# Optimization experiments

Hardware: AMD Instinct MI355X
Metric: run time of the kernel (lower is better)

Reference implementation:

```python
import jax, jax.numpy as jnp
import numpy as np
from jax import lax

B, N, M, C = 32, 4096, 256, 91
EPS = 1e-7  # torchvision giou_loss eps
NEG_INF = -jnp.inf


def _make_boxes(key, b, n):
    # valid xyxy boxes in [0,1]
    kc, ks = jax.random.split(key)
    c = jax.random.uniform(kc, (b, n, 2), minval=0.1, maxval=0.9)
    wh = jax.random.uniform(ks, (b, n, 2), minval=0.02, maxval=0.2)
    return jnp.concatenate([c - wh / 2, c + wh / 2], axis=-1)


def setup_inputs() -> dict:
    key = jax.random.key(0)
    k1, k2, k3, k4 = jax.random.split(key, 4)
    return {
        "pr_boxes": _make_boxes(k1, B, N),
        "gt_boxes": _make_boxes(k2, B, M),
        "pr_class_logits": jax.random.normal(k3, (B, N, C), dtype=jnp.float32),
        "gt_classes": jax.random.randint(k4, (B, M), 0, C),
    }


def _box_iou(a, b):
    # a: [N,4], b: [M,4] xyxy -> [N,M] (torchvision.ops.box_iou)
    lt = jnp.maximum(a[:, None, :2], b[None, :, :2])
    rb = jnp.minimum(a[:, None, 2:], b[None, :, 2:])
    wh = jnp.clip(rb - lt, 0.0)
    inter = wh[..., 0] * wh[..., 1]
    area_a = (a[:, 2] - a[:, 0]) * (a[:, 3] - a[:, 1])
    area_b = (b[:, 2] - b[:, 0]) * (b[:, 3] - b[:, 1])
    union = area_a[:, None] + area_b[None, :] - inter
    return inter / union


def _match(pr, gt):
    # greedy maximal-IoU matching: sequentially take global argmax, mask row+col
    ious = _box_iou(pr, gt)  # [N, M]

    def step(ious, _):
        idx = jnp.argmax(ious)
        i, j = idx // M, idx % M
        ious = ious.at[i, :].set(NEG_INF).at[:, j].set(NEG_INF)
        return ious, (i, j)

    _, (pr_idx, gt_order) = lax.scan(step, ious, None, length=M)
    pr_mask = jnp.zeros((N,), dtype=bool).at[pr_idx].set(True)
    return pr_idx, gt_order, pr_mask


def _giou_loss_mean(b1, b2):
    # elementwise generalized_box_iou_loss, reduction='mean' (torchvision)
    xi1 = jnp.maximum(b1[:, 0], b2[:, 0])
    yi1 = jnp.maximum(b1[:, 1], b2[:, 1])
    xi2 = jnp.minimum(b1[:, 2], b2[:, 2])
    yi2 = jnp.minimum(b1[:, 3], b2[:, 3])
    inter = jnp.clip(xi2 - xi1, 0.0) * jnp.clip(yi2 - yi1, 0.0)
    area1 = (b1[:, 2] - b1[:, 0]) * (b1[:, 3] - b1[:, 1])
    area2 = (b2[:, 2] - b2[:, 0]) * (b2[:, 3] - b2[:, 1])
    union = area1 + area2 - inter
    iou = inter / (union + EPS)
    xc1 = jnp.minimum(b1[:, 0], b2[:, 0])
    yc1 = jnp.minimum(b1[:, 1], b2[:, 1])
    xc2 = jnp.maximum(b1[:, 2], b2[:, 2])
    yc2 = jnp.maximum(b1[:, 3], b2[:, 3])
    area_c = (xc2 - xc1) * (yc2 - yc1)
    giou = iou - (area_c - union) / (area_c + EPS)
    return jnp.mean(1.0 - giou)


def reference(pr_boxes, gt_boxes, pr_class_logits, gt_classes):
    pr_idx, gt_order, pr_mask = jax.vmap(_match)(pr_boxes, gt_boxes)  # [B,M],[B,M],[B,N]
    # unmatched prediction indices (fixed count N-M)
    neg_idx = jax.vmap(lambda m: jnp.nonzero(~m, size=N - M)[0])(pr_mask)  # [B, N-M]

    pr_pos = jnp.take_along_axis(pr_boxes, pr_idx[..., None], axis=1)   # [B,M,4]
    gt_pos = jnp.take_along_axis(gt_boxes, gt_order[..., None], axis=1)  # [B,M,4]
    pr_neg = jnp.take_along_axis(pr_boxes, neg_idx[..., None], axis=1)  # [B,N-M,4]
    gt_neg = jnp.zeros_like(pr_neg)

    l_loss = (jax.vmap(_giou_loss_mean)(pr_pos, gt_pos).sum()
              + jax.vmap(_giou_loss_mean)(pr_neg, gt_neg).sum())
    # c_loss is never accumulated in the original module (classification branch is dead code)
    c_loss = 0.0
    count = pr_boxes.shape[0]
    return (c_loss + l_loss) / count / 2.0
```

## Files before the change

### kernel.cpp

```cpp
#include <hip/hip_runtime.h>

#pragma clang fp contract(off)

#define NBOX 4096
#define MBOX 256
#define NBATCH 32
#define GEPS 1e-7f
#define DEPTH 12
#define RDEPTH 8

typedef unsigned long long u64;
typedef unsigned int u32;
typedef unsigned short u16;

#define OFF_PRS   0
#define OFF_TOP   65536
#define OFF_G     90112
#define OFF_GAR   94208
#define OFF_MATCH 95232
#define LDS_BYTES 96256

__device__ __forceinline__ u64 shfl_u64(u64 x, int src) {
  u32 lo = (u32)x, hi = (u32)(x >> 32);
  lo = __shfl(lo, src, 64);
  hi = __shfl(hi, src, 64);
  return ((u64)hi << 32) | (u64)lo;
}

__device__ __forceinline__ u32 wave_max_u32(u32 x) {
#define DPPL32(CTRL)                                                            \
  {                                                                             \
    u32 s = (u32)__builtin_amdgcn_update_dpp(0, (int)x, CTRL, 0xf, 0xf, true);  \
    x = x > s ? x : s;                                                          \
  }
  DPPL32(0xB1) DPPL32(0x4E) DPPL32(0x141) DPPL32(0x140) DPPL32(0x142) DPPL32(0x143)
#undef DPPL32
  return (u32)__builtin_amdgcn_readlane((int)x, 63);
}

__device__ __forceinline__ u64 wave_max_colkey(u64 key) {
  u32 iou = (u32)(key >> 13);
  u32 maxiou = wave_max_u32(iou);
  u32 tb = (iou == maxiou) ? ((u32)key & 0x1FFFu) : 0u;
  u32 maxtb = wave_max_u32(tb);
  return ((u64)maxiou << 13) | (u64)maxtb;
}

__device__ __forceinline__ u32 iou_bits(float4 a, float areaA, float4 g, float gar) {
  #pragma clang fp contract(off)
  float w = fminf(a.z, g.z) - fmaxf(a.x, g.x);
  float h = fminf(a.w, g.w) - fmaxf(a.y, g.y);
  w = fmaxf(w, 0.0f);
  h = fmaxf(h, 0.0f);
  float inter = w * h;
  float uni = (areaA + gar) - inter;
  float v = inter / uni;
  return __float_as_uint(v);
}

__device__ __forceinline__ float giou_loss(float ax1, float ay1, float ax2, float ay2,
                                           float bx1, float by1, float bx2, float by2) {
  #pragma clang fp contract(off)
  float xi1 = fmaxf(ax1, bx1), yi1 = fmaxf(ay1, by1);
  float xi2 = fminf(ax2, bx2), yi2 = fminf(ay2, by2);
  float inter = fmaxf(xi2 - xi1, 0.0f) * fmaxf(yi2 - yi1, 0.0f);
  float area1 = (ax2 - ax1) * (ay2 - ay1);
  float area2 = (bx2 - bx1) * (by2 - by1);
  float uni = (area1 + area2) - inter;
  float iou = inter / (uni + GEPS);
  float xc1 = fminf(ax1, bx1), yc1 = fminf(ay1, by1);
  float xc2 = fmaxf(ax2, bx2), yc2 = fmaxf(ay2, by2);
  float areac = (xc2 - xc1) * (yc2 - yc1);
  float giou = iou - (areac - uni) / (areac + GEPS);
  return 1.0f - giou;
}


__global__ __launch_bounds__(256) __attribute__((amdgpu_waves_per_eu(1, 6)))
void init_cols(const float4* __restrict__ pr, const float4* __restrict__ gt,
               u64* __restrict__ topG) {
  const int blk = blockIdx.x;
  const int b = blk >> 6, cg = blk & 63;
  const int tid = threadIdx.x, lane = tid & 63, wid = tid >> 6;
  const int j = cg * 4 + wid;
  const float4* prb = pr + (size_t)b * NBOX;
  float4 gb = gt[(size_t)b * MBOX + j];
  float gar = (gb.z - gb.x) * (gb.w - gb.y);

  u64 t0 = 0ull, t1 = 0ull, t2 = 0ull, dm = 0ull;
  for (int k = 0; k < 64; ++k) {
    int r = (k << 6) + lane;
    float4 a = prb[r];
    float areaA = (a.z - a.x) * (a.w - a.y);
    u64 key = ((u64)iou_bits(a, areaA, gb, gar) << 13) | (u64)(NBOX - r);
    bool c0 = key > t0, c1 = key > t1, c2 = key > t2;
    u64 d = c2 ? t2 : key;
    if (d > dm) dm = d;
    u64 n1 = c1 ? (c0 ? t0 : key) : t1;
    u64 n2 = c2 ? (c1 ? t1 : key) : t2;
    t0 = c0 ? key : t0;
    t1 = n1;
    t2 = n2;
  }
  u64* out = topG + ((size_t)b * MBOX + j) * DEPTH;
  int h = 0;
  u64 m12 = 0ull;
  for (int e = 0; e < DEPTH; ++e) {
    u64 cand = (h == 0) ? t0 : (h == 1) ? t1 : (h == 2) ? t2 : 0ull;
    u64 m = wave_max_colkey(cand);
    if (cand == m && m) h++;
    if (lane == 0) out[e] = m;
    m12 = m;
  }
  if (__ballot(dm > m12) != 0ull) {
    u64 t[DEPTH];
    #pragma unroll
    for (int q = 0; q < DEPTH; ++q) t[q] = 0ull;
    for (int k = 0; k < 64; ++k) {
      int r = (k << 6) + lane;
      float4 a = prb[r];
      float areaA = (a.z - a.x) * (a.w - a.y);
      u64 key = ((u64)iou_bits(a, areaA, gb, gar) << 13) | (u64)(NBOX - r);
      if (key > t[DEPTH - 1]) {
        t[DEPTH - 1] = key;
        #pragma unroll
        for (int q = DEPTH - 1; q > 0; --q)
          if (t[q] > t[q - 1]) { u64 tmp = t[q]; t[q] = t[q - 1]; t[q - 1] = tmp; }
      }
    }
    int h2 = 0;
    for (int e = 0; e < DEPTH; ++e) {
      u64 cand = 0;
      #pragma unroll
      for (int q = 0; q < DEPTH; ++q) if (q == h2) cand = t[q];
      u64 m = wave_max_colkey(cand);
      if (cand == m && m) h2++;
      if (lane == 0) out[e] = m;
    }
  }
}

__global__ __launch_bounds__(64) __attribute__((amdgpu_waves_per_eu(1, 4)))
void greedy_kernel(const float4* __restrict__ pr, const float4* __restrict__ gt,
                   const u64* __restrict__ topG, float* __restrict__ partial) {
  extern __shared__ char smem[];
  float4* prs  = (float4*)(smem + OFF_PRS);
  u64* top     = (u64*)(smem + OFF_TOP);
  float4* g    = (float4*)(smem + OFF_G);
  float* garea = (float*)(smem + OFF_GAR);
  u32* match   = (u32*)(smem + OFF_MATCH);

  const int b = blockIdx.x;
  const int lane = threadIdx.x;
  const float4* prb = pr + (size_t)b * NBOX;

  float negdiff = 0.0f, possum = 0.0f, negsub = 0.0f;
  for (int k = 0; k < 64; ++k) {
    int r = (k << 6) + lane;
    float4 a = prb[r];
    prs[r] = a;
    negdiff += giou_loss(a.x, a.y, a.z, a.w, 0.0f, 0.0f, 0.0f, 0.0f);
  }
  #pragma unroll
  for (int k = 0; k < 4; ++k) {
    int j = (k << 6) + lane;
    float4 gg = gt[(size_t)b * MBOX + j];
    g[j] = gg;
    garea[j] = (gg.z - gg.x) * (gg.w - gg.y);
  }
  {
    float4* dst = (float4*)top;
    const float4* src = (const float4*)(topG + (size_t)b * MBOX * DEPTH);
    for (int k = 0; k < MBOX * DEPTH / 2 / 64; ++k) dst[(k << 6) + lane] = src[(k << 6) + lane];
  }
  u64 rowlive = ~0ull;
  u64 cb[4];
  u64 la[4];
  u64 cfc[4];
  u32 posreg = 0x02020202u;
  #pragma unroll
  for (int q = 0; q < 4; ++q) {
    int j = (q << 6) + lane;
    cfc[q] = (u64)(MBOX - j);
    u64 e0 = top[j * DEPTH];
    u64 e1 = top[j * DEPTH + 1];
    cb[q] = ((e0 >> 13) << 22) | ((e0 & 0x1FFFull) << 9) | cfc[q];
    la[q] = e1;
  }

  for (int step = 0; step < MBOX; ++step) {
    u64 m0 = cb[0] > cb[1] ? cb[0] : cb[1];
    u64 m1 = cb[2] > cb[3] ? cb[2] : cb[3];
    u64 mb = m0 > m1 ? m0 : m1;
    u32 iou32 = (u32)(mb >> 22);
    u32 maxiou = wave_max_u32(iou32);
    u32 tb = (iou32 == maxiou) ? ((u32)mb & 0x3FFFFFu) : 0u;
    u32 maxtb = wave_max_u32(tb);
    if (lane == 0) match[step] = maxtb;
    if (step == MBOX - 1) break;
    const u32 rfield = (maxtb >> 9) & 0x1FFFu;
    const int i = NBOX - (int)rfield;
    u64 kill = (lane == (i & 63)) ? (1ull << (i >> 6)) : 0ull;
    rowlive &= ~kill;
    u32 walkmask = 0;
    #pragma unroll
    for (int q = 0; q < 4; ++q) {
      u32 lo22 = (u32)cb[q] & 0x3FFFFFu;
      bool aff = (lo22 >> 9) == rfield;
      bool ismatch = (lo22 == maxtb);
      if (aff && ismatch) cb[q] = 0ull;
      if (aff && !ismatch) walkmask |= (1u << q);
    }
    u64 wb = __ballot(walkmask != 0);
    if (wb != 0ull) {
      u32 need = walkmask;
      u32 exmask = 0;
      for (;;) {
        #pragma unroll
        for (int q = 0; q < 4; ++q) {
          u64 e = la[q];
          int r = NBOX - (int)(e & 0x1FFFull);
          u64 rl = shfl_u64(rowlive, r & 63);
          if ((need >> q) & 1) {
            if (e == 0ull) {
              cb[q] = 0ull;
              need &= ~(1u << q);
              exmask |= (1u << q);
            } else if ((rl >> ((r >> 6) & 63)) & 1ull) {
              cb[q] = ((e >> 13) << 22) | ((e & 0x1FFFull) << 9) | cfc[q];
              need &= ~(1u << q);
              int p = (int)((posreg >> (q * 8)) & 0xFFu);
              la[q] = (p < DEPTH) ? top[((q << 6) + lane) * DEPTH + p] : 0ull;
              posreg = (posreg & ~(0xFFu << (q * 8))) | ((u32)(p + 1) << (q * 8));
            } else {
              int p = (int)((posreg >> (q * 8)) & 0xFFu);
              la[q] = (p < DEPTH) ? top[((q << 6) + lane) * DEPTH + p] : 0ull;
              posreg = (posreg & ~(0xFFu << (q * 8))) | ((u32)(p + 1) << (q * 8));
            }
          }
        }
        if (__ballot(need != 0) == 0ull) break;
      }
      u64 exb = __ballot(exmask != 0);
      while (exb != 0ull) {
        const int src = (int)__ffsll((unsigned long long)exb) - 1;
        const u32 em = (u32)__shfl((int)exmask, src, 64);
        const int q = __ffs(em) - 1;
        const int jj = (q << 6) + src;
        if (lane == src) exmask &= ~(1u << q);
        exb = __ballot(exmask != 0);
        float4 gb = g[jj];
        float gar = garea[jj];
        u64 t[RDEPTH];
        #pragma unroll
        for (int z = 0; z < RDEPTH; ++z) t[z] = 0ull;
        for (int k = 0; k < 64; ++k) {
          if ((rowlive >> k) & 1ull) {
            int rr = (k << 6) + lane;
            float4 a = prs[rr];
            float areaA = (a.z - a.x) * (a.w - a.y);
            u64 key = ((u64)iou_bits(a, areaA, gb, gar) << 13) | (u64)(NBOX - rr);
            if (key > t[RDEPTH - 1]) {
              t[RDEPTH - 1] = key;
              #pragma unroll
              for (int z = RDEPTH - 1; z > 0; --z)
                if (t[z] > t[z - 1]) { u64 tmp = t[z]; t[z] = t[z - 1]; t[z - 1] = tmp; }
            }
          }
        }
        u64 ent0 = 0ull, ent1 = 0ull;
        int h = 0;
        for (int e = 0; e < RDEPTH; ++e) {
          u64 cand = 0;
          #pragma unroll
          for (int z = 0; z < RDEPTH; ++z) if (z == h) cand = t[z];
          u64 mm = wave_max_colkey(cand);
          if (cand == mm && mm) h++;
          if (e == 0) ent0 = mm;
          if (e == 1) ent1 = mm;
          if (lane == 0) top[jj * DEPTH + e] = mm;
        }
        if (lane >= RDEPTH && lane < DEPTH) top[jj * DEPTH + lane] = 0ull;
        if (lane == src) {
          cb[q] = ((ent0 >> 13) << 22) | ((ent0 & 0x1FFFull) << 9) | cfc[q];
          la[q] = ent1;
          posreg = (posreg & ~(0xFFu << (q * 8))) | (2u << (q * 8));
        }
      }
    }
  }

  #pragma unroll
  for (int t4 = 0; t4 < 4; ++t4) {
    int s = (t4 << 6) + lane;
    u32 mm = match[s];
    int i = NBOX - (int)(mm >> 9);
    int j = MBOX - (int)(mm & 0x1FFu);
    float4 a = prs[i];
    float4 gg = g[j];
    possum += giou_loss(a.x, a.y, a.z, a.w, gg.x, gg.y, gg.z, gg.w);
    negsub += giou_loss(a.x, a.y, a.z, a.w, 0.0f, 0.0f, 0.0f, 0.0f);
  }

  #pragma unroll
  for (int o = 32; o; o >>= 1) {
    possum  += __shfl_xor(possum, o, 64);
    negsub  += __shfl_xor(negsub, o, 64);
    negdiff += __shfl_xor(negdiff, o, 64);
  }
  if (lane == 0)
    partial[b] = possum / 256.0f + (negdiff - negsub) / 3840.0f;
}

__global__ void finalize_kernel(const float* __restrict__ partial, float* __restrict__ out) {
  if (threadIdx.x == 0) {
    float s = 0.0f;
    for (int i = 0; i < NBATCH; ++i) s += partial[i];
    out[0] = s / 64.0f;
  }
}

extern "C" void kernel_launch(void* const* d_in, const int* in_sizes, int n_in,
                              void* d_out, int out_size, void* d_ws, size_t ws_size,
                              hipStream_t stream) {
  (void)in_sizes; (void)n_in; (void)out_size; (void)ws_size;
  const float4* pr = (const float4*)d_in[0];
  const float4* gt = (const float4*)d_in[1];
  char* ws = (char*)d_ws;
  u64* topG = (u64*)ws;
  float* partial = (float*)(ws + (size_t)NBATCH * MBOX * DEPTH * 8);
  float* out = (float*)d_out;

  hipFuncSetAttribute((const void*)greedy_kernel,
                      hipFuncAttributeMaxDynamicSharedMemorySize, LDS_BYTES);

  hipLaunchKernelGGL(init_cols, dim3(NBATCH * 64), dim3(256), 0, stream, pr, gt, topG);
  hipLaunchKernelGGL(greedy_kernel, dim3(NBATCH), dim3(64), LDS_BYTES, stream,
                     pr, gt, topG, partial);
  hipLaunchKernelGGL(finalize_kernel, dim3(1), dim3(64), 0, stream, partial, out);
}
```

Before: 167.2 us.

## Deepen column top-list, fast-path unique argmax, fuse finalize via atomics

Raises the per-column candidate list depth from 12 to 16 (the fallback full-sort path keeps depth 12 and zero-pads the rest), so fewer refills are needed during greedy matching. In the greedy step, the second wave-wide max reduction is replaced by a ballot plus readlane when only one lane holds the maximum IoU. The separate finalize kernel is removed: each block adds its partial to a fixed-point 64-bit atomic accumulator and the last block writes the output. The column scan is unrolled by 4. This adds a memset launch and more LDS per block.

```diff
diff --git a/kernel.cpp b/kernel.cpp
--- a/kernel.cpp
+++ b/kernel.cpp
@@ -6,7 +6,8 @@
 #define MBOX 256
 #define NBATCH 32
 #define GEPS 1e-7f
-#define DEPTH 12
+#define DEPTH 16
+#define FDEPTH 12
 #define RDEPTH 8
 
 typedef unsigned long long u64;
@@ -15,10 +16,10 @@
 
 #define OFF_PRS   0
 #define OFF_TOP   65536
-#define OFF_G     90112
-#define OFF_GAR   94208
-#define OFF_MATCH 95232
-#define LDS_BYTES 96256
+#define OFF_G     98304
+#define OFF_GAR   102400
+#define OFF_MATCH 103424
+#define LDS_BYTES 104448
 
 __device__ __forceinline__ u64 shfl_u64(u64 x, int src) {
   u32 lo = (u32)x, hi = (u32)(x >> 32);
@@ -88,6 +89,7 @@
   float gar = (gb.z - gb.x) * (gb.w - gb.y);
 
   u64 t0 = 0ull, t1 = 0ull, t2 = 0ull, dm = 0ull;
+  #pragma unroll 4
   for (int k = 0; k < 64; ++k) {
     int r = (k << 6) + lane;
     float4 a = prb[r];
@@ -104,45 +106,50 @@
   }
   u64* out = topG + ((size_t)b * MBOX + j) * DEPTH;
   int h = 0;
-  u64 m12 = 0ull;
+  u64 mlast = 0ull;
   for (int e = 0; e < DEPTH; ++e) {
     u64 cand = (h == 0) ? t0 : (h == 1) ? t1 : (h == 2) ? t2 : 0ull;
     u64 m = wave_max_colkey(cand);
     if (cand == m && m) h++;
     if (lane == 0) out[e] = m;
-    m12 = m;
-  }
-  if (__ballot(dm > m12) != 0ull) {
-    u64 t[DEPTH];
+    mlast = m;
+  }
+  if (__ballot(dm > mlast) != 0ull) {
+    u64 t[FDEPTH];
     #pragma unroll
-    for (int q = 0; q < DEPTH; ++q) t[q] = 0ull;
+    for (int q = 0; q < FDEPTH; ++q) t[q] = 0ull;
     for (int k = 0; k < 64; ++k) {
       int r = (k << 6) + lane;
       float4 a = prb[r];
       float areaA = (a.z - a.x) * (a.w - a.y);
       u64 key = ((u64)iou_bits(a, areaA, gb, gar) << 13) | (u64)(NBOX - r);
-      if (key > t[DEPTH - 1]) {
-        t[DEPTH - 1] = key;
+      if (key > t[FDEPTH - 1]) {
+        t[FDEPTH - 1] = key;
         #pragma unroll
-        for (int q = DEPTH - 1; q > 0; --q)
+        for (int q = FDEPTH - 1; q > 0; --q)
           if (t[q] > t[q - 1]) { u64 tmp = t[q]; t[q] = t[q - 1]; t[q - 1] = tmp; }
       }
     }
     int h2 = 0;
-    for (int e = 0; e < DEPTH; ++e) {
+    for (int e = 0; e < FDEPTH; ++e) {
       u64 cand = 0;
       #pragma unroll
-      for (int q = 0; q < DEPTH; ++q) if (q == h2) cand = t[q];
+      for (int q = 0; q < FDEPTH; ++q) if (q == h2) cand = t[q];
       u64 m = wave_max_colkey(cand);
       if (cand == m && m) h2++;
       if (lane == 0) out[e] = m;
     }
+    if (lane == 0) {
+      #pragma unroll
+      for (int e = FDEPTH; e < DEPTH; ++e) out[e] = 0ull;
+    }
   }
 }
 
 __global__ __launch_bounds__(64) __attribute__((amdgpu_waves_per_eu(1, 4)))
 void greedy_kernel(const float4* __restrict__ pr, const float4* __restrict__ gt,
-                   const u64* __restrict__ topG, float* __restrict__ partial) {
+                   const u64* __restrict__ topG, unsigned long long* __restrict__ acc,
+                   unsigned int* __restrict__ cnt, float* __restrict__ out) {
   extern __shared__ char smem[];
   float4* prs  = (float4*)(smem + OFF_PRS);
   u64* top     = (u64*)(smem + OFF_TOP);
@@ -194,8 +201,16 @@
     u64 mb = m0 > m1 ? m0 : m1;
     u32 iou32 = (u32)(mb >> 22);
     u32 maxiou = wave_max_u32(iou32);
-    u32 tb = (iou32 == maxiou) ? ((u32)mb & 0x3FFFFFu) : 0u;
-    u32 maxtb = wave_max_u32(tb);
+    u32 mytb = (u32)mb & 0x3FFFFFu;
+    u64 eq = __ballot(iou32 == maxiou && mb != 0ull);
+    u32 maxtb;
+    if (__popcll(eq) == 1) {
+      int l = (int)__ffsll((unsigned long long)eq) - 1;
+      maxtb = (u32)__builtin_amdgcn_readlane((int)mytb, l);
+    } else {
+      u32 tbv = (iou32 == maxiou && mb != 0ull) ? mytb : 0u;
+      maxtb = wave_max_u32(tbv);
+    }
     if (lane == 0) match[step] = maxtb;
     if (step == MBOX - 1) break;
     const u32 rfield = (maxtb >> 9) & 0x1FFFu;
@@ -308,15 +323,17 @@
     negsub  += __shfl_xor(negsub, o, 64);
     negdiff += __shfl_xor(negdiff, o, 64);
   }
-  if (lane == 0)
-    partial[b] = possum / 256.0f + (negdiff - negsub) / 3840.0f;
-}
-
-__global__ void finalize_kernel(const float* __restrict__ partial, float* __restrict__ out) {
-  if (threadIdx.x == 0) {
-    float s = 0.0f;
-    for (int i = 0; i < NBATCH; ++i) s += partial[i];
-    out[0] = s / 64.0f;
+  if (lane == 0) {
+    float pb = possum / 256.0f + (negdiff - negsub) / 3840.0f;
+    long long fx = (long long)llrint((double)pb * 4294967296.0);
+    atomicAdd(acc, (unsigned long long)fx);
+    __threadfence();
+    unsigned int c = atomicAdd(cnt, 1u);
+    if (c == NBATCH - 1) {
+      unsigned long long raw = atomicAdd(acc, 0ull);
+      double s = (double)(long long)raw / 4294967296.0;
+      out[0] = (float)(s / 64.0);
+    }
   }
 }
 
@@ -328,14 +345,15 @@
   const float4* gt = (const float4*)d_in[1];
   char* ws = (char*)d_ws;
   u64* topG = (u64*)ws;
-  float* partial = (float*)(ws + (size_t)NBATCH * MBOX * DEPTH * 8);
+  unsigned long long* acc = (unsigned long long*)(ws + (size_t)NBATCH * MBOX * DEPTH * 8);
+  unsigned int* cnt = (unsigned int*)(ws + (size_t)NBATCH * MBOX * DEPTH * 8 + 8);
   float* out = (float*)d_out;
 
   hipFuncSetAttribute((const void*)greedy_kernel,
                       hipFuncAttributeMaxDynamicSharedMemorySize, LDS_BYTES);
 
+  hipMemsetAsync(acc, 0, 16, stream);
   hipLaunchKernelGGL(init_cols, dim3(NBATCH * 64), dim3(256), 0, stream, pr, gt, topG);
   hipLaunchKernelGGL(greedy_kernel, dim3(NBATCH), dim3(64), LDS_BYTES, stream,
-                     pr, gt, topG, partial);
-  hipLaunchKernelGGL(finalize_kernel, dim3(1), dim3(64), 0, stream, partial, out);
-}
+                     pr, gt, topG, acc, cnt, out);
+}
```

Result: slower. 177.1 us (+5.9%).
